# Kernel optimization log

Measured on AMD Instinct MI355X. Metric: run time of the kernel, lower is better.

The kernel has to match this reference:

```python
import jax, jax.numpy as jnp
import numpy as np

N = 50000      # nodes
E = 800000     # edges (before self-loops)
F = 128        # num_features
H = 64         # hidden_channels
B = 512        # batch_size (num graphs)
NC = 10        # num_classes


def setup_inputs() -> dict:
    key = jax.random.key(0)
    ks = jax.random.split(key, 24)
    rn = lambda k, shp, s=0.05: jax.random.normal(k, shp, jnp.float32) * s
    inp = {}
    inp["x"] = jax.random.normal(ks[0], (N, F), jnp.float32)
    inp["edge_index"] = jax.random.randint(ks[1], (2, E), 0, N)
    inp["batch"] = jnp.sort(jax.random.randint(ks[2], (N,), 0, B))
    # GATConv1: in F -> 4 heads x H (concat)
    inp["W1"] = rn(ks[3], (F, 4 * H)); inp["a_src1"] = rn(ks[4], (4, H))
    inp["a_dst1"] = rn(ks[5], (4, H)); inp["b1"] = rn(ks[6], (4 * H,))
    # GATConv2: in 4H -> 1 head x 2H
    inp["W2"] = rn(ks[7], (4 * H, 2 * H)); inp["a_src2"] = rn(ks[8], (1, 2 * H))
    inp["a_dst2"] = rn(ks[9], (1, 2 * H)); inp["b2"] = rn(ks[10], (2 * H,))
    # GCNConv: in 2H -> H
    inp["Wg"] = rn(ks[11], (2 * H, H)); inp["bg"] = rn(ks[12], (H,))
    # BatchNorms (eval mode: running_mean=0, running_var=1)
    inp["bn1_g"] = 1.0 + rn(ks[13], (4 * H,)); inp["bn1_b"] = rn(ks[14], (4 * H,))
    inp["bn2_g"] = 1.0 + rn(ks[15], (2 * H,)); inp["bn2_b"] = rn(ks[16], (2 * H,))
    inp["bn3_g"] = 1.0 + rn(ks[17], (2 * H,)); inp["bn3_b"] = rn(ks[18], (2 * H,))
    inp["lin1_W"] = rn(ks[19], (H, 128)); inp["lin1_b"] = rn(ks[20], (128,))
    inp["lin2_W"] = rn(ks[21], (128, NC)); inp["lin2_b"] = rn(ks[22], (NC,))
    inp["batch_size"] = B
    return inp


def _gat(x, src, dst, W, a_s, a_d, b, n):
    """PyG GATConv (eval): project, edge attention (leaky_relu 0.2), dst-softmax, scatter."""
    heads, ch = a_s.shape
    h = (x @ W).reshape(n, heads, ch)                       # [N, heads, ch]
    sc_s = (h * a_s).sum(-1)                                # [N, heads]
    sc_d = (h * a_d).sum(-1)
    e = jax.nn.leaky_relu(sc_s[src] + sc_d[dst], 0.2)       # [E2, heads]
    m = jax.ops.segment_max(e, dst, num_segments=n)
    ee = jnp.exp(e - m[dst])
    s = jax.ops.segment_sum(ee, dst, num_segments=n)
    alpha = ee / (s[dst] + 1e-16)                           # edge softmax per dst
    out = jax.ops.segment_sum(h[src] * alpha[:, :, None], dst, num_segments=n)
    return out.reshape(n, heads * ch) + b


def _bn_eval(x, g, b, eps=1e-5):
    # BatchNorm1d eval with running_mean=0, running_var=1
    return x * (g / jnp.sqrt(1.0 + eps)) + b


def reference(x, edge_index, batch, W1, a_src1, a_dst1, b1, W2, a_src2, a_dst2, b2,
              Wg, bg, bn1_g, bn1_b, bn2_g, bn2_b, bn3_g, bn3_b,
              lin1_W, lin1_b, lin2_W, lin2_b, batch_size):
    n = x.shape[0]
    loop = jnp.arange(n)
    src = jnp.concatenate([edge_index[0], loop])            # add self-loops (PyG default)
    dst = jnp.concatenate([edge_index[1], loop])
    lrelu = lambda v: jax.nn.leaky_relu(v, 0.01)            # module's LeakyReLU()

    x1 = _bn_eval(lrelu(_gat(x, src, dst, W1, a_src1, a_dst1, b1, n)), bn1_g, bn1_b)
    x2 = _bn_eval(lrelu(_gat(x1, src, dst, W2, a_src2, a_dst2, b2, n)), bn2_g, bn2_b)

    # GCNConv with symmetric normalization over A + I
    deg = jax.ops.segment_sum(jnp.ones_like(dst, jnp.float32), dst, num_segments=n)
    dis = jnp.where(deg > 0, jax.lax.rsqrt(deg), 0.0)
    h = x2 @ Wg                                             # [N, H]
    msg = h[src] * (dis[src] * dis[dst])[:, None]
    x3 = lrelu(jax.ops.segment_sum(msg, dst, num_segments=n) + bg)

    # global_mean_pool over graphs (dropout is identity in eval)
    sums = jax.ops.segment_sum(x3, batch, num_segments=batch_size)
    cnt = jax.ops.segment_sum(jnp.ones((n,), jnp.float32), batch, num_segments=batch_size)
    pooled = sums / jnp.clip(cnt, 1.0)[:, None]             # [B, H]

    y = lrelu(_bn_eval(pooled @ lin1_W + lin1_b, bn3_g, bn3_b))
    return y @ lin2_W + lin2_b                              # [B, NC]
```

## Files before the change

### kernel.cpp

```cpp
#include <hip/hip_runtime.h>
#include <hip/hip_bf16.h>

#define NN  50000
#define EE  800000
#define NE2 850000
#define NB  512
#define NRT 3125
#define NSB 196

#define BN_RS 0.9999950000374997f

typedef __attribute__((ext_vector_type(8))) short short8;
typedef __attribute__((ext_vector_type(4))) float f32x4;

__device__ __forceinline__ float bf2f(__hip_bfloat16 v) { return __bfloat162float(v); }
__device__ __forceinline__ unsigned short f2b(float v) {
    __hip_bfloat16 b = __float2bfloat16(v);
    return *reinterpret_cast<unsigned short*>(&b);
}
__device__ __forceinline__ float u2f(unsigned short u) {
    union { unsigned u; float f; } c; c.u = ((unsigned)u) << 16; return c.f;
}
__device__ __forceinline__ float4 u42f4(ushort4 v) {
    float4 r; r.x = u2f(v.x); r.y = u2f(v.y); r.z = u2f(v.z); r.w = u2f(v.w); return r;
}
__device__ __forceinline__ float lrelu01(float v) { return v > 0.f ? v : 0.01f * v; }
__device__ __forceinline__ float lrelu02(float v) { return v > 0.f ? v : 0.2f * v; }

__device__ __forceinline__ void edge_sd(const int* __restrict__ ei, int e, int& s, int& d) {
    if (e < EE) { s = ei[e]; d = ei[EE + e]; }
    else        { s = e - EE; d = e - EE; }
}

__device__ __forceinline__ float ldf(const void* p, int i, bool bf) {
    return bf ? bf2f(((const __hip_bfloat16*)p)[i]) : ((const float*)p)[i];
}

__global__ __launch_bounds__(256) void det_k(const unsigned* __restrict__ xw, int* __restrict__ flag) {
    __shared__ int cnt;
    if (threadIdx.x == 0) cnt = 0;
    __syncthreads();
    int c = 0;
#pragma unroll
    for (int k = 0; k < 4; ++k) {
        unsigned w = xw[threadIdx.x * 4 + k];
        unsigned ef = (w >> 7) & 0xFFu;
        if (ef >= 100u && ef <= 140u) c++;
    }
    atomicAdd(&cnt, c);
    __syncthreads();
    if (threadIdx.x == 0) *flag = (cnt > 512) ? 1 : 0;
}

#define NSEG 20
#define WTOT 85578
#define XQUADS (NN * 32)
#define PREP_TOT (XQUADS + WTOT + 32768 + 32768 + 8192)
struct SegArgs { const void* src[NSEG]; int off[NSEG]; };

__global__ __launch_bounds__(256) void prep_k(SegArgs a,
                                              const void* __restrict__ x_raw,
                                              ushort4* __restrict__ xb4,
                                              const void* __restrict__ W1r,
                                              const void* __restrict__ W2r,
                                              const void* __restrict__ Wgr,
                                              float* __restrict__ wf,
                                              unsigned short* __restrict__ W1t,
                                              unsigned short* __restrict__ W2t,
                                              unsigned short* __restrict__ Wgt,
                                              const int* __restrict__ flag) {
    bool bf = (*flag != 0);
    int i = blockIdx.x * 256 + threadIdx.x;
    if (i >= PREP_TOT) return;
    if (i < XQUADS) {
        ushort4 o;
        if (bf) o = ((const ushort4*)x_raw)[i];
        else {
            float4 v = ((const float4*)x_raw)[i];
            o.x = f2b(v.x); o.y = f2b(v.y); o.z = f2b(v.z); o.w = f2b(v.w);
        }
        xb4[i] = o;
        return;
    }
    i -= XQUADS;
    if (i < WTOT) {
        int s = 0;
#pragma unroll
        for (int k = 1; k < NSEG; ++k) if (i >= a.off[k]) s = k;
        wf[i] = ldf(a.src[s], i - a.off[s], bf);
        return;
    }
    i -= WTOT;
    if (i < 32768) {
        int n = i >> 7, k = i & 127;
        W1t[i] = f2b(ldf(W1r, k * 256 + n, bf));
        return;
    }
    i -= 32768;
    if (i < 32768) {
        int n = i >> 8, k = i & 255;
        W2t[i] = f2b(ldf(W2r, k * 128 + n, bf));
        return;
    }
    i -= 32768;
    {
        int n = i >> 7, k = i & 127;
        Wgt[i] = f2b(ldf(Wgr, k * 64 + n, bf));
    }
}

__global__ __launch_bounds__(256) void deg_k(const int* __restrict__ ei, int* __restrict__ degi) {
    int e = blockIdx.x * 256 + threadIdx.x;
    if (e >= NE2) return;
    int s, d; edge_sd(ei, e, s, d);
    atomicAdd(&degi[d], 1);
}

__global__ __launch_bounds__(256) void pscan_k(const int* __restrict__ degi,
                                               int* __restrict__ incl, int* __restrict__ bsum) {
    __shared__ int tmp[256];
    int t = threadIdx.x;
    int i = blockIdx.x * 256 + t;
    int v = (i < NN) ? degi[i] : 0;
    tmp[t] = v;
    __syncthreads();
#pragma unroll
    for (int off = 1; off < 256; off <<= 1) {
        int u = (t >= off) ? tmp[t - off] : 0;
        __syncthreads();
        tmp[t] += u;
        __syncthreads();
    }
    if (i < NN) incl[i] = tmp[t];
    if (t == 255) bsum[blockIdx.x] = tmp[255];
}

__global__ __launch_bounds__(256) void bscan_k(int* __restrict__ bsum) {
    __shared__ int tmp[256];
    int t = threadIdx.x;
    tmp[t] = (t < NSB) ? bsum[t] : 0;
    __syncthreads();
#pragma unroll
    for (int off = 1; off < 256; off <<= 1) {
        int u = (t >= off) ? tmp[t - off] : 0;
        __syncthreads();
        tmp[t] += u;
        __syncthreads();
    }
    if (t < NSB) bsum[t] = tmp[t];
}

__global__ __launch_bounds__(256) void fscan_k(const int* __restrict__ degi,
                                               const int* __restrict__ incl,
                                               const int* __restrict__ bsum,
                                               int* __restrict__ row_ptr, int* __restrict__ cursor,
                                               float* __restrict__ dis) {
    int i = blockIdx.x * 256 + threadIdx.x;
    if (i >= NN) return;
    int dg = degi[i];
    int base = (blockIdx.x > 0) ? bsum[blockIdx.x - 1] : 0;
    int ex = base + incl[i] - dg;
    row_ptr[i] = ex; cursor[i] = ex;
    dis[i] = dg > 0 ? rsqrtf((float)dg) : 0.f;
    if (i == NN - 1) row_ptr[NN] = bsum[NSB - 1];
}

__global__ __launch_bounds__(256) void scatter_k(const int* __restrict__ ei,
                                                 int* __restrict__ cursor,
                                                 int* __restrict__ csr_src) {
    int e = blockIdx.x * 256 + threadIdx.x;
    if (e >= NE2) return;
    int s, d; edge_sd(ei, e, s, d);
    int pos = atomicAdd(&cursor[d], 1);
    csr_src[pos] = s;
}

__global__ __launch_bounds__(256) void mgemm1_k(const short* __restrict__ A,
                                                const short* __restrict__ Bt,
                                                unsigned short* __restrict__ C,
                                                const float* __restrict__ a_s,
                                                const float* __restrict__ a_d,
                                                float* __restrict__ sc_s,
                                                float* __restrict__ sc_d) {
    int wave = threadIdx.x >> 6, lane = threadIdx.x & 63;
    int rt = blockIdx.x, cg = wave;
    int l15 = lane & 15, quad = lane >> 4;
    const short* ap = A + (size_t)(rt * 16 + l15) * 128 + quad * 8;
    const short* bp = Bt + (size_t)(cg * 64 + l15) * 128 + quad * 8;
    f32x4 acc[4] = {};
    for (int k0 = 0; k0 < 128; k0 += 32) {
        short8 a = *(const short8*)(ap + k0);
#pragma unroll
        for (int j = 0; j < 4; ++j) {
            short8 b = *(const short8*)(bp + (size_t)j * 16 * 128 + k0);
            acc[j] = __builtin_amdgcn_mfma_f32_16x16x32_bf16(a, b, acc[j], 0, 0, 0);
        }
    }
    float asv[4], adv[4];
#pragma unroll
    for (int j = 0; j < 4; ++j) {
        asv[j] = a_s[cg * 64 + j * 16 + l15];
        adv[j] = a_d[cg * 64 + j * 16 + l15];
    }
    float ss[4] = {0.f, 0.f, 0.f, 0.f}, sd[4] = {0.f, 0.f, 0.f, 0.f};
#pragma unroll
    for (int j = 0; j < 4; ++j) {
        int n = cg * 64 + j * 16 + l15;
#pragma unroll
        for (int r = 0; r < 4; ++r) {
            float v = acc[j][r];
            C[(size_t)(rt * 16 + quad * 4 + r) * 256 + n] = f2b(v);
            ss[r] = fmaf(v, asv[j], ss[r]);
            sd[r] = fmaf(v, adv[j], sd[r]);
        }
    }
#pragma unroll
    for (int off = 1; off < 16; off <<= 1) {
#pragma unroll
        for (int r = 0; r < 4; ++r) {
            ss[r] += __shfl_xor(ss[r], off);
            sd[r] += __shfl_xor(sd[r], off);
        }
    }
    if (l15 == 0) {
#pragma unroll
        for (int r = 0; r < 4; ++r) {
            int node = rt * 16 + quad * 4 + r;
            sc_s[node * 4 + cg] = ss[r];
            sc_d[node * 4 + cg] = sd[r];
        }
    }
}

__global__ __launch_bounds__(256) void mgemm2_k(const short* __restrict__ A,
                                                const short* __restrict__ Bt,
                                                unsigned short* __restrict__ C,
                                                const float* __restrict__ a_s,
                                                const float* __restrict__ a_d,
                                                float* __restrict__ sc_s,
                                                float* __restrict__ sc_d) {
    __shared__ float sred[4][16][2];
    int wave = threadIdx.x >> 6, lane = threadIdx.x & 63;
    int gidx = blockIdx.x * 4 + wave;
    bool act = gidx < NRT * 2;
    int gcl = act ? gidx : NRT * 2 - 1;
    int rt = gcl >> 1, cg = gcl & 1;
    int l15 = lane & 15, quad = lane >> 4;
    const short* ap = A + (size_t)(rt * 16 + l15) * 256 + quad * 8;
    const short* bp = Bt + (size_t)(cg * 64 + l15) * 256 + quad * 8;
    f32x4 acc[4] = {};
    for (int k0 = 0; k0 < 256; k0 += 32) {
        short8 a = *(const short8*)(ap + k0);
#pragma unroll
        for (int j = 0; j < 4; ++j) {
            short8 b = *(const short8*)(bp + (size_t)j * 16 * 256 + k0);
            acc[j] = __builtin_amdgcn_mfma_f32_16x16x32_bf16(a, b, acc[j], 0, 0, 0);
        }
    }
    float asv[4], adv[4];
#pragma unroll
    for (int j = 0; j < 4; ++j) {
        asv[j] = a_s[cg * 64 + j * 16 + l15];
        adv[j] = a_d[cg * 64 + j * 16 + l15];
    }
    float ss[4] = {0.f, 0.f, 0.f, 0.f}, sd[4] = {0.f, 0.f, 0.f, 0.f};
#pragma unroll
    for (int j = 0; j < 4; ++j) {
        int n = cg * 64 + j * 16 + l15;
#pragma unroll
        for (int r = 0; r < 4; ++r) {
            float v = acc[j][r];
            if (act) C[(size_t)(rt * 16 + quad * 4 + r) * 128 + n] = f2b(v);
            ss[r] = fmaf(v, asv[j], ss[r]);
            sd[r] = fmaf(v, adv[j], sd[r]);
        }
    }
#pragma unroll
    for (int off = 1; off < 16; off <<= 1) {
#pragma unroll
        for (int r = 0; r < 4; ++r) {
            ss[r] += __shfl_xor(ss[r], off);
            sd[r] += __shfl_xor(sd[r], off);
        }
    }
    if (l15 == 0) {
#pragma unroll
        for (int r = 0; r < 4; ++r) {
            sred[wave][quad * 4 + r][0] = ss[r];
            sred[wave][quad * 4 + r][1] = sd[r];
        }
    }
    __syncthreads();
    if (threadIdx.x < 32) {
        int rl = threadIdx.x >> 4, row = threadIdx.x & 15;
        int g2 = blockIdx.x * 4 + rl * 2;
        if (g2 < NRT * 2) {
            int node = (g2 >> 1) * 16 + row;
            sc_s[node] = sred[rl * 2][row][0] + sred[rl * 2 + 1][row][0];
            sc_d[node] = sred[rl * 2][row][1] + sred[rl * 2 + 1][row][1];
        }
    }
}

__global__ __launch_bounds__(256) void mgemm3_k(const short* __restrict__ A,
                                                const short* __restrict__ Bt,
                                                unsigned short* __restrict__ C) {
    int wave = threadIdx.x >> 6, lane = threadIdx.x & 63;
    int gidx = blockIdx.x * 4 + wave;
    if (gidx >= NRT) return;
    int rt = gidx;
    int l15 = lane & 15, quad = lane >> 4;
    const short* ap = A + (size_t)(rt * 16 + l15) * 128 + quad * 8;
    const short* bp = Bt + (size_t)l15 * 128 + quad * 8;
    f32x4 acc[4] = {};
    for (int k0 = 0; k0 < 128; k0 += 32) {
        short8 a = *(const short8*)(ap + k0);
#pragma unroll
        for (int j = 0; j < 4; ++j) {
            short8 b = *(const short8*)(bp + (size_t)j * 16 * 128 + k0);
            acc[j] = __builtin_amdgcn_mfma_f32_16x16x32_bf16(a, b, acc[j], 0, 0, 0);
        }
    }
#pragma unroll
    for (int j = 0; j < 4; ++j) {
        int n = j * 16 + l15;
#pragma unroll
        for (int r = 0; r < 4; ++r)
            C[(size_t)(rt * 16 + quad * 4 + r) * 64 + n] = f2b(acc[j][r]);
    }
}

__device__ __forceinline__ float sel4(float4 v, int head) {
    float ab = (head & 1) ? v.y : v.x;
    float cd = (head & 1) ? v.w : v.z;
    return (head & 2) ? cd : ab;
}

__global__ __launch_bounds__(256) void agg1_k(const int* __restrict__ row_ptr,
                                              const int* __restrict__ csr_src,
                                              const ushort4* __restrict__ h1b,
                                              const float4* __restrict__ sc_s4,
                                              const float4* __restrict__ sc_d4,
                                              const float4* __restrict__ b1,
                                              const float4* __restrict__ g1,
                                              const float4* __restrict__ bb1,
                                              ushort4* __restrict__ x1b) {
    int n = __builtin_amdgcn_readfirstlane((blockIdx.x * 256 + threadIdx.x) >> 6);
    int lane = threadIdx.x & 63;
    if (n >= NN) return;
    int row = row_ptr[n], end = row_ptr[n + 1];
    int head = lane >> 4;
    float scd_h = sel4(sc_d4[n], head);
    float4 acc = {0.f, 0.f, 0.f, 0.f};
    float den = 0.f;
    int c = row;
    for (; c + 3 < end; c += 4) {
        int s0 = csr_src[c], s1 = csr_src[c + 1], s2 = csr_src[c + 2], s3 = csr_src[c + 3];
        float4 scs0 = sc_s4[s0], scs1 = sc_s4[s1], scs2 = sc_s4[s2], scs3 = sc_s4[s3];
        float4 hv0 = u42f4(h1b[(size_t)s0 * 64 + lane]);
        float4 hv1 = u42f4(h1b[(size_t)s1 * 64 + lane]);
        float4 hv2 = u42f4(h1b[(size_t)s2 * 64 + lane]);
        float4 hv3 = u42f4(h1b[(size_t)s3 * 64 + lane]);
        float e0 = __expf(lrelu02(sel4(scs0, head) + scd_h));
        float e1 = __expf(lrelu02(sel4(scs1, head) + scd_h));
        float e2 = __expf(lrelu02(sel4(scs2, head) + scd_h));
        float e3 = __expf(lrelu02(sel4(scs3, head) + scd_h));
        den += (e0 + e1) + (e2 + e3);
        acc.x = fmaf(hv0.x, e0, fmaf(hv1.x, e1, fmaf(hv2.x, e2, fmaf(hv3.x, e3, acc.x))));
        acc.y = fmaf(hv0.y, e0, fmaf(hv1.y, e1, fmaf(hv2.y, e2, fmaf(hv3.y, e3, acc.y))));
        acc.z = fmaf(hv0.z, e0, fmaf(hv1.z, e1, fmaf(hv2.z, e2, fmaf(hv3.z, e3, acc.z))));
        acc.w = fmaf(hv0.w, e0, fmaf(hv1.w, e1, fmaf(hv2.w, e2, fmaf(hv3.w, e3, acc.w))));
    }
    for (; c < end; ++c) {
        int s0 = csr_src[c];
        float4 scs0 = sc_s4[s0];
        float4 hv0 = u42f4(h1b[(size_t)s0 * 64 + lane]);
        float e0 = __expf(lrelu02(sel4(scs0, head) + scd_h));
        den += e0;
        acc.x = fmaf(hv0.x, e0, acc.x);
        acc.y = fmaf(hv0.y, e0, acc.y);
        acc.z = fmaf(hv0.z, e0, acc.z);
        acc.w = fmaf(hv0.w, e0, acc.w);
    }
    float inv = 1.f / (den + 1e-16f);
    float4 bb = b1[lane], gg = g1[lane], be = bb1[lane];
    ushort4 o;
    o.x = f2b(lrelu01(acc.x * inv + bb.x) * (gg.x * BN_RS) + be.x);
    o.y = f2b(lrelu01(acc.y * inv + bb.y) * (gg.y * BN_RS) + be.y);
    o.z = f2b(lrelu01(acc.z * inv + bb.z) * (gg.z * BN_RS) + be.z);
    o.w = f2b(lrelu01(acc.w * inv + bb.w) * (gg.w * BN_RS) + be.w);
    x1b[(size_t)n * 64 + lane] = o;
}

__global__ __launch_bounds__(256) void agg2_k(const int* __restrict__ row_ptr,
                                              const int* __restrict__ csr_src,
                                              const ushort4* __restrict__ h2b,
                                              const float* __restrict__ sc_s,
                                              const float* __restrict__ sc_d,
                                              const float4* __restrict__ b2,
                                              const float4* __restrict__ g2,
                                              const float4* __restrict__ bb2,
                                              ushort4* __restrict__ x2b) {
    int n = __builtin_amdgcn_readfirstlane((blockIdx.x * 256 + threadIdx.x) >> 6);
    int lane = threadIdx.x & 63;
    if (n >= NN) return;
    int g = lane >> 5, sl = lane & 31;
    int row = row_ptr[n], end = row_ptr[n + 1];
    float scd = sc_d[n];
    float4 acc = {0.f, 0.f, 0.f, 0.f};
    float den = 0.f;
    int c = row + g;
    for (; c + 2 < end; c += 4) {
        int s0 = csr_src[c], s1 = csr_src[c + 2];
        float sc0 = sc_s[s0], sc1 = sc_s[s1];
        float4 hv0 = u42f4(h2b[(size_t)s0 * 32 + sl]);
        float4 hv1 = u42f4(h2b[(size_t)s1 * 32 + sl]);
        float e0 = __expf(lrelu02(sc0 + scd));
        float e1 = __expf(lrelu02(sc1 + scd));
        den += e0 + e1;
        acc.x = fmaf(hv0.x, e0, fmaf(hv1.x, e1, acc.x));
        acc.y = fmaf(hv0.y, e0, fmaf(hv1.y, e1, acc.y));
        acc.z = fmaf(hv0.z, e0, fmaf(hv1.z, e1, acc.z));
        acc.w = fmaf(hv0.w, e0, fmaf(hv1.w, e1, acc.w));
    }
    if (c < end) {
        int s0 = csr_src[c];
        float e0 = __expf(lrelu02(sc_s[s0] + scd));
        float4 hv0 = u42f4(h2b[(size_t)s0 * 32 + sl]);
        den += e0;
        acc.x = fmaf(hv0.x, e0, acc.x);
        acc.y = fmaf(hv0.y, e0, acc.y);
        acc.z = fmaf(hv0.z, e0, acc.z);
        acc.w = fmaf(hv0.w, e0, acc.w);
    }
    den += __shfl_xor(den, 32);
    acc.x += __shfl_xor(acc.x, 32);
    acc.y += __shfl_xor(acc.y, 32);
    acc.z += __shfl_xor(acc.z, 32);
    acc.w += __shfl_xor(acc.w, 32);
    if (g == 0) {
        float inv = 1.f / (den + 1e-16f);
        float4 bb = b2[sl], gg = g2[sl], be = bb2[sl];
        ushort4 o;
        o.x = f2b(lrelu01(acc.x * inv + bb.x) * (gg.x * BN_RS) + be.x);
        o.y = f2b(lrelu01(acc.y * inv + bb.y) * (gg.y * BN_RS) + be.y);
        o.z = f2b(lrelu01(acc.z * inv + bb.z) * (gg.z * BN_RS) + be.z);
        o.w = f2b(lrelu01(acc.w * inv + bb.w) * (gg.w * BN_RS) + be.w);
        x2b[(size_t)n * 32 + sl] = o;
    }
}

__global__ __launch_bounds__(256) void gcn_k(const int* __restrict__ row_ptr,
                                             const int* __restrict__ csr_src,
                                             const ushort4* __restrict__ hgb,
                                             const float* __restrict__ dis,
                                             const float4* __restrict__ bg,
                                             float4* __restrict__ x3) {
    int n = __builtin_amdgcn_readfirstlane((blockIdx.x * 256 + threadIdx.x) >> 6);
    int lane = threadIdx.x & 63;
    if (n >= NN) return;
    int g = lane >> 4, sl = lane & 15;
    int row = row_ptr[n], end = row_ptr[n + 1];
    float dn = dis[n];
    float4 acc = {0.f, 0.f, 0.f, 0.f};
    int c = row + g;
    for (; c + 4 < end; c += 8) {
        int s0 = csr_src[c], s1 = csr_src[c + 4];
        float w0 = dis[s0], w1 = dis[s1];
        float4 hv0 = u42f4(hgb[(size_t)s0 * 16 + sl]);
        float4 hv1 = u42f4(hgb[(size_t)s1 * 16 + sl]);
        acc.x = fmaf(hv0.x, w0, fmaf(hv1.x, w1, acc.x));
        acc.y = fmaf(hv0.y, w0, fmaf(hv1.y, w1, acc.y));
        acc.z = fmaf(hv0.z, w0, fmaf(hv1.z, w1, acc.z));
        acc.w = fmaf(hv0.w, w0, fmaf(hv1.w, w1, acc.w));
    }
    if (c < end) {
        int s0 = csr_src[c];
        float w0 = dis[s0];
        float4 hv0 = u42f4(hgb[(size_t)s0 * 16 + sl]);
        acc.x = fmaf(hv0.x, w0, acc.x);
        acc.y = fmaf(hv0.y, w0, acc.y);
        acc.z = fmaf(hv0.z, w0, acc.z);
        acc.w = fmaf(hv0.w, w0, acc.w);
    }
#pragma unroll
    for (int off = 16; off <= 32; off <<= 1) {
        acc.x += __shfl_xor(acc.x, off);
        acc.y += __shfl_xor(acc.y, off);
        acc.z += __shfl_xor(acc.z, off);
        acc.w += __shfl_xor(acc.w, off);
    }
    if (g == 0) {
        float4 bb = bg[sl];
        float4 o;
        o.x = lrelu01(acc.x * dn + bb.x);
        o.y = lrelu01(acc.y * dn + bb.y);
        o.z = lrelu01(acc.z * dn + bb.z);
        o.w = lrelu01(acc.w * dn + bb.w);
        x3[(size_t)n * 16 + sl] = o;
    }
}

__global__ __launch_bounds__(1024) void bounds_k(const int* __restrict__ batch, int* __restrict__ gstart) {
    int t = threadIdx.x;
    if (t > NB) return;
    int lo = 0, hi = NN;
    while (lo < hi) { int mid = (lo + hi) >> 1; if (batch[mid] < t) lo = mid + 1; else hi = mid; }
    gstart[t] = lo;
}

__global__ __launch_bounds__(256) void pool_k(const float* __restrict__ x3,
                                              const int* __restrict__ gstart,
                                              float* __restrict__ pooled) {
    __shared__ float red[4][64];
    int g = blockIdx.x, t = threadIdx.x;
    int c = t & 63, r = t >> 6;
    int s = gstart[g], e = gstart[g + 1];
    float sum = 0.f;
    for (int n = s + r; n < e; n += 4) sum += x3[(size_t)n * 64 + c];
    red[r][c] = sum;
    __syncthreads();
    if (t < 64) {
        float v = red[0][t] + red[1][t] + red[2][t] + red[3][t];
        int cnt = e - s; if (cnt < 1) cnt = 1;
        pooled[g * 64 + t] = v / (float)cnt;
    }
}

__global__ __launch_bounds__(128) void mlp_k(const float* __restrict__ pooled,
                                             const float* __restrict__ l1W,
                                             const float* __restrict__ l1b,
                                             const float* __restrict__ g3,
                                             const float* __restrict__ b3,
                                             const float* __restrict__ l2W,
                                             const float* __restrict__ l2b,
                                             void* __restrict__ outp,
                                             const int* __restrict__ flag) {
    __shared__ float pl[64];
    __shared__ float y1s[128];
    int g = blockIdx.x, t = threadIdx.x;
    if (t < 64) pl[t] = pooled[g * 64 + t];
    __syncthreads();
    float acc = l1b[t];
#pragma unroll 8
    for (int j = 0; j < 64; ++j) acc = fmaf(pl[j], l1W[j * 128 + t], acc);
    acc = acc * (g3[t] * BN_RS) + b3[t];
    y1s[t] = lrelu01(acc);
    __syncthreads();
    if (t < 10) {
        float o = l2b[t];
#pragma unroll 8
        for (int j = 0; j < 128; ++j) o = fmaf(y1s[j], l2W[j * 10 + t], o);
        if (*flag) ((__hip_bfloat16*)outp)[g * 10 + t] = __float2bfloat16(o);
        else       ((float*)outp)[g * 10 + t] = o;
    }
}

static const int kSegN[NSEG]  = {32768, 256, 256, 256, 32768, 128, 128, 128, 8192, 64,
                                 256, 256, 128, 128, 128, 128, 8192, 128, 1280, 10};
static const int kSegIn[NSEG] = {3, 4, 5, 6, 7, 8, 9, 10, 11, 12, 13, 14, 15, 16, 17, 18, 19, 20, 21, 22};

extern "C" void kernel_launch(void* const* d_in, const int* in_sizes, int n_in,
                              void* d_out, int out_size, void* d_ws, size_t ws_size,
                              hipStream_t stream) {
    const void* x_raw = d_in[0];
    const int*  ei    = (const int*)d_in[1];
    const int*  batch = (const int*)d_in[2];

    int*   flag = (int*)d_ws;
    float* ws   = (float*)d_ws;
    unsigned short* xb = (unsigned short*)(ws + 16);
    float* wf   = ws + 16 + (size_t)NN * 64;
    unsigned short* W1t = (unsigned short*)(wf + 85584);
    unsigned short* W2t = W1t + 32768;
    unsigned short* Wgt = W2t + 32768;
    unsigned short* h1b = Wgt + 8192;
    unsigned short* x1b = h1b + (size_t)NN * 256;
    unsigned short* x2b = x1b + (size_t)NN * 256;
    unsigned short* hgb = x2b + (size_t)NN * 128;
    float* x3   = (float*)(hgb + (size_t)NN * 64);
    float* sc_s1 = x3 + (size_t)NN * 64;
    float* sc_d1 = sc_s1 + (size_t)NN * 4;
    float* sc_s2 = sc_d1 + (size_t)NN * 4;
    float* sc_d2 = sc_s2 + NN;
    float* disb  = sc_d2 + NN;
    float* pooled = disb + NN;
    int*   gstart = (int*)(pooled + NB * 64);
    int*   degi   = gstart + NB + 4;
    int*   incl   = degi + NN;
    int*   bsum   = incl + NN;
    int*   row_ptr = bsum + 256;
    int*   cursor  = row_ptr + NN + 1;
    int*   csr_src = cursor + NN;

    int off[NSEG]; int o = 0;
    for (int s = 0; s < NSEG; ++s) { off[s] = o; o += kSegN[s]; }
    float* as1f = wf + off[1];  float* ad1f = wf + off[2];
    float* b1f  = wf + off[3];  float* as2f = wf + off[5];
    float* ad2f = wf + off[6];  float* b2f  = wf + off[7];
    float* bgf  = wf + off[9];  float* bn1g = wf + off[10]; float* bn1b = wf + off[11];
    float* bn2g = wf + off[12]; float* bn2b = wf + off[13]; float* bn3g = wf + off[14];
    float* bn3b = wf + off[15]; float* l1Wf = wf + off[16]; float* l1bf = wf + off[17];
    float* l2Wf = wf + off[18]; float* l2bf = wf + off[19];

    unsigned short* h2b = h1b;

    det_k<<<1, 256, 0, stream>>>((const unsigned*)x_raw, flag);
    SegArgs sa;
    for (int s = 0; s < NSEG; ++s) { sa.src[s] = d_in[kSegIn[s]]; sa.off[s] = off[s]; }
    prep_k<<<(PREP_TOT + 255) / 256, 256, 0, stream>>>(sa, x_raw, (ushort4*)xb,
                                                       d_in[3], d_in[7], d_in[11],
                                                       wf, W1t, W2t, Wgt, flag);

    hipMemsetAsync(degi, 0, NN * sizeof(int), stream);
    deg_k<<<(NE2 + 255) / 256, 256, 0, stream>>>(ei, degi);
    pscan_k<<<NSB, 256, 0, stream>>>(degi, incl, bsum);
    bscan_k<<<1, 256, 0, stream>>>(bsum);
    fscan_k<<<NSB, 256, 0, stream>>>(degi, incl, bsum, row_ptr, cursor, disb);
    scatter_k<<<(NE2 + 255) / 256, 256, 0, stream>>>(ei, cursor, csr_src);
    bounds_k<<<1, 1024, 0, stream>>>(batch, gstart);

    mgemm1_k<<<NRT, 256, 0, stream>>>((const short*)xb, (const short*)W1t, h1b,
                                      as1f, ad1f, sc_s1, sc_d1);
    agg1_k<<<12500, 256, 0, stream>>>(row_ptr, csr_src, (const ushort4*)h1b,
                                      (const float4*)sc_s1, (const float4*)sc_d1,
                                      (const float4*)b1f, (const float4*)bn1g,
                                      (const float4*)bn1b, (ushort4*)x1b);

    mgemm2_k<<<(NRT * 2 + 3) / 4, 256, 0, stream>>>((const short*)x1b, (const short*)W2t, h2b,
                                                    as2f, ad2f, sc_s2, sc_d2);
    agg2_k<<<12500, 256, 0, stream>>>(row_ptr, csr_src, (const ushort4*)h2b,
                                      sc_s2, sc_d2,
                                      (const float4*)b2f, (const float4*)bn2g,
                                      (const float4*)bn2b, (ushort4*)x2b);

    mgemm3_k<<<(NRT + 3) / 4, 256, 0, stream>>>((const short*)x2b, (const short*)Wgt, hgb);
    gcn_k<<<12500, 256, 0, stream>>>(row_ptr, csr_src, (const ushort4*)hgb, disb,
                                     (const float4*)bgf, (float4*)x3);
    pool_k<<<NB, 256, 0, stream>>>(x3, gstart, pooled);

    mlp_k<<<NB, 128, 0, stream>>>(pooled, l1Wf, l1bf, bn3g, bn3b, l2Wf, l2bf, d_out, flag);
}
```

Baseline: 458.9 us.

## Fold setup kernels into prep and fscan, deepen gather unrolling in aggregations

Merges the dtype-detection kernel and the degree memset into prep_k: every block recomputes the bf16 detection locally and also zeroes degi. It moves the graph-boundary binary search into fscan_k, which cuts three launches. The aggregation loops in agg1/agg2/gcn now issue more independent gathers per iteration, giving more memory-level parallelism. In exchange, every prep block repeats the 1024-word detection read, and the wider unroll raises register pressure.

Measured after the change: 455.9 us. No clear change (-0.6%).

```diff
diff --git a/kernel.cpp b/kernel.cpp
--- a/kernel.cpp
+++ b/kernel.cpp
@@ -36,26 +36,10 @@
     return bf ? bf2f(((const __hip_bfloat16*)p)[i]) : ((const float*)p)[i];
 }
 
-__global__ __launch_bounds__(256) void det_k(const unsigned* __restrict__ xw, int* __restrict__ flag) {
-    __shared__ int cnt;
-    if (threadIdx.x == 0) cnt = 0;
-    __syncthreads();
-    int c = 0;
-#pragma unroll
-    for (int k = 0; k < 4; ++k) {
-        unsigned w = xw[threadIdx.x * 4 + k];
-        unsigned ef = (w >> 7) & 0xFFu;
-        if (ef >= 100u && ef <= 140u) c++;
-    }
-    atomicAdd(&cnt, c);
-    __syncthreads();
-    if (threadIdx.x == 0) *flag = (cnt > 512) ? 1 : 0;
-}
-
 #define NSEG 20
 #define WTOT 85578
 #define XQUADS (NN * 32)
-#define PREP_TOT (XQUADS + WTOT + 32768 + 32768 + 8192)
+#define PREP_TOT (NN + XQUADS + WTOT + 32768 + 32768 + 8192)
 struct SegArgs { const void* src[NSEG]; int off[NSEG]; };
 
 __global__ __launch_bounds__(256) void prep_k(SegArgs a,
@@ -68,10 +52,31 @@
                                               unsigned short* __restrict__ W1t,
                                               unsigned short* __restrict__ W2t,
                                               unsigned short* __restrict__ Wgt,
-                                              const int* __restrict__ flag) {
-    bool bf = (*flag != 0);
-    int i = blockIdx.x * 256 + threadIdx.x;
+                                              int* __restrict__ degi,
+                                              int* __restrict__ flag) {
+    __shared__ int cnt;
+    int t = threadIdx.x;
+    if (t == 0) cnt = 0;
+    __syncthreads();
+    {
+        int c = 0;
+        const unsigned* xw = (const unsigned*)x_raw;
+#pragma unroll
+        for (int k = 0; k < 4; ++k) {
+            unsigned w = xw[t * 4 + k];
+            unsigned ef = (w >> 7) & 0xFFu;
+            if (ef >= 100u && ef <= 140u) c++;
+        }
+        atomicAdd(&cnt, c);
+    }
+    __syncthreads();
+    bool bf = (cnt > 512);
+    if (blockIdx.x == 0 && t == 0) *flag = bf ? 1 : 0;
+
+    int i = blockIdx.x * 256 + t;
     if (i >= PREP_TOT) return;
+    if (i < NN) { degi[i] = 0; return; }
+    i -= NN;
     if (i < XQUADS) {
         ushort4 o;
         if (bf) o = ((const ushort4*)x_raw)[i];
@@ -153,9 +158,15 @@
 __global__ __launch_bounds__(256) void fscan_k(const int* __restrict__ degi,
                                                const int* __restrict__ incl,
                                                const int* __restrict__ bsum,
+                                               const int* __restrict__ batch,
                                                int* __restrict__ row_ptr, int* __restrict__ cursor,
-                                               float* __restrict__ dis) {
+                                               float* __restrict__ dis, int* __restrict__ gstart) {
     int i = blockIdx.x * 256 + threadIdx.x;
+    if (i <= NB) {
+        int lo = 0, hi = NN;
+        while (lo < hi) { int mid = (lo + hi) >> 1; if (batch[mid] < i) lo = mid + 1; else hi = mid; }
+        gstart[i] = lo;
+    }
     if (i >= NN) return;
     int dg = degi[i];
     int base = (blockIdx.x > 0) ? bsum[blockIdx.x - 1] : 0;
@@ -354,22 +365,48 @@
     float4 acc = {0.f, 0.f, 0.f, 0.f};
     float den = 0.f;
     int c = row;
+    for (; c + 7 < end; c += 8) {
+        int s[8];
+#pragma unroll
+        for (int j = 0; j < 8; ++j) s[j] = csr_src[c + j];
+        float4 scs[8];
+#pragma unroll
+        for (int j = 0; j < 8; ++j) scs[j] = sc_s4[s[j]];
+        ushort4 hu[8];
+#pragma unroll
+        for (int j = 0; j < 8; ++j) hu[j] = h1b[(size_t)s[j] * 64 + lane];
+        float e[8];
+#pragma unroll
+        for (int j = 0; j < 8; ++j) { e[j] = __expf(lrelu02(sel4(scs[j], head) + scd_h)); den += e[j]; }
+#pragma unroll
+        for (int j = 0; j < 8; ++j) {
+            float4 hv = u42f4(hu[j]);
+            acc.x = fmaf(hv.x, e[j], acc.x);
+            acc.y = fmaf(hv.y, e[j], acc.y);
+            acc.z = fmaf(hv.z, e[j], acc.z);
+            acc.w = fmaf(hv.w, e[j], acc.w);
+        }
+    }
     for (; c + 3 < end; c += 4) {
-        int s0 = csr_src[c], s1 = csr_src[c + 1], s2 = csr_src[c + 2], s3 = csr_src[c + 3];
-        float4 scs0 = sc_s4[s0], scs1 = sc_s4[s1], scs2 = sc_s4[s2], scs3 = sc_s4[s3];
-        float4 hv0 = u42f4(h1b[(size_t)s0 * 64 + lane]);
-        float4 hv1 = u42f4(h1b[(size_t)s1 * 64 + lane]);
-        float4 hv2 = u42f4(h1b[(size_t)s2 * 64 + lane]);
-        float4 hv3 = u42f4(h1b[(size_t)s3 * 64 + lane]);
-        float e0 = __expf(lrelu02(sel4(scs0, head) + scd_h));
-        float e1 = __expf(lrelu02(sel4(scs1, head) + scd_h));
-        float e2 = __expf(lrelu02(sel4(scs2, head) + scd_h));
-        float e3 = __expf(lrelu02(sel4(scs3, head) + scd_h));
-        den += (e0 + e1) + (e2 + e3);
-        acc.x = fmaf(hv0.x, e0, fmaf(hv1.x, e1, fmaf(hv2.x, e2, fmaf(hv3.x, e3, acc.x))));
-        acc.y = fmaf(hv0.y, e0, fmaf(hv1.y, e1, fmaf(hv2.y, e2, fmaf(hv3.y, e3, acc.y))));
-        acc.z = fmaf(hv0.z, e0, fmaf(hv1.z, e1, fmaf(hv2.z, e2, fmaf(hv3.z, e3, acc.z))));
-        acc.w = fmaf(hv0.w, e0, fmaf(hv1.w, e1, fmaf(hv2.w, e2, fmaf(hv3.w, e3, acc.w))));
+        int s[4];
+#pragma unroll
+        for (int j = 0; j < 4; ++j) s[j] = csr_src[c + j];
+        float4 scs[4];
+#pragma unroll
+        for (int j = 0; j < 4; ++j) scs[j] = sc_s4[s[j]];
+        ushort4 hu[4];
+#pragma unroll
+        for (int j = 0; j < 4; ++j) hu[j] = h1b[(size_t)s[j] * 64 + lane];
+#pragma unroll
+        for (int j = 0; j < 4; ++j) {
+            float e0 = __expf(lrelu02(sel4(scs[j], head) + scd_h));
+            den += e0;
+            float4 hv = u42f4(hu[j]);
+            acc.x = fmaf(hv.x, e0, acc.x);
+            acc.y = fmaf(hv.y, e0, acc.y);
+            acc.z = fmaf(hv.z, e0, acc.z);
+            acc.w = fmaf(hv.w, e0, acc.w);
+        }
     }
     for (; c < end; ++c) {
         int s0 = csr_src[c];
@@ -410,20 +447,28 @@
     float4 acc = {0.f, 0.f, 0.f, 0.f};
     float den = 0.f;
     int c = row + g;
-    for (; c + 2 < end; c += 4) {
-        int s0 = csr_src[c], s1 = csr_src[c + 2];
-        float sc0 = sc_s[s0], sc1 = sc_s[s1];
-        float4 hv0 = u42f4(h2b[(size_t)s0 * 32 + sl]);
-        float4 hv1 = u42f4(h2b[(size_t)s1 * 32 + sl]);
-        float e0 = __expf(lrelu02(sc0 + scd));
-        float e1 = __expf(lrelu02(sc1 + scd));
-        den += e0 + e1;
-        acc.x = fmaf(hv0.x, e0, fmaf(hv1.x, e1, acc.x));
-        acc.y = fmaf(hv0.y, e0, fmaf(hv1.y, e1, acc.y));
-        acc.z = fmaf(hv0.z, e0, fmaf(hv1.z, e1, acc.z));
-        acc.w = fmaf(hv0.w, e0, fmaf(hv1.w, e1, acc.w));
-    }
-    if (c < end) {
+    for (; c + 6 < end; c += 8) {
+        int s[4];
+#pragma unroll
+        for (int j = 0; j < 4; ++j) s[j] = csr_src[c + 2 * j];
+        float sc[4];
+#pragma unroll
+        for (int j = 0; j < 4; ++j) sc[j] = sc_s[s[j]];
+        ushort4 hu[4];
+#pragma unroll
+        for (int j = 0; j < 4; ++j) hu[j] = h2b[(size_t)s[j] * 32 + sl];
+#pragma unroll
+        for (int j = 0; j < 4; ++j) {
+            float e0 = __expf(lrelu02(sc[j] + scd));
+            den += e0;
+            float4 hv = u42f4(hu[j]);
+            acc.x = fmaf(hv.x, e0, acc.x);
+            acc.y = fmaf(hv.y, e0, acc.y);
+            acc.z = fmaf(hv.z, e0, acc.z);
+            acc.w = fmaf(hv.w, e0, acc.w);
+        }
+    }
+    for (; c < end; c += 2) {
         int s0 = csr_src[c];
         float e0 = __expf(lrelu02(sc_s[s0] + scd));
         float4 hv0 = u42f4(h2b[(size_t)s0 * 32 + sl]);
@@ -464,17 +509,26 @@
     float dn = dis[n];
     float4 acc = {0.f, 0.f, 0.f, 0.f};
     int c = row + g;
-    for (; c + 4 < end; c += 8) {
-        int s0 = csr_src[c], s1 = csr_src[c + 4];
-        float w0 = dis[s0], w1 = dis[s1];
-        float4 hv0 = u42f4(hgb[(size_t)s0 * 16 + sl]);
-        float4 hv1 = u42f4(hgb[(size_t)s1 * 16 + sl]);
-        acc.x = fmaf(hv0.x, w0, fmaf(hv1.x, w1, acc.x));
-        acc.y = fmaf(hv0.y, w0, fmaf(hv1.y, w1, acc.y));
-        acc.z = fmaf(hv0.z, w0, fmaf(hv1.z, w1, acc.z));
-        acc.w = fmaf(hv0.w, w0, fmaf(hv1.w, w1, acc.w));
-    }
-    if (c < end) {
+    for (; c + 12 < end; c += 16) {
+        int s[4];
+#pragma unroll
+        for (int j = 0; j < 4; ++j) s[j] = csr_src[c + 4 * j];
+        float w[4];
+#pragma unroll
+        for (int j = 0; j < 4; ++j) w[j] = dis[s[j]];
+        ushort4 hu[4];
+#pragma unroll
+        for (int j = 0; j < 4; ++j) hu[j] = hgb[(size_t)s[j] * 16 + sl];
+#pragma unroll
+        for (int j = 0; j < 4; ++j) {
+            float4 hv = u42f4(hu[j]);
+            acc.x = fmaf(hv.x, w[j], acc.x);
+            acc.y = fmaf(hv.y, w[j], acc.y);
+            acc.z = fmaf(hv.z, w[j], acc.z);
+            acc.w = fmaf(hv.w, w[j], acc.w);
+        }
+    }
+    for (; c < end; c += 4) {
         int s0 = csr_src[c];
         float w0 = dis[s0];
         float4 hv0 = u42f4(hgb[(size_t)s0 * 16 + sl]);
@@ -499,14 +553,6 @@
         o.w = lrelu01(acc.w * dn + bb.w);
         x3[(size_t)n * 16 + sl] = o;
     }
-}
-
-__global__ __launch_bounds__(1024) void bounds_k(const int* __restrict__ batch, int* __restrict__ gstart) {
-    int t = threadIdx.x;
-    if (t > NB) return;
-    int lo = 0, hi = NN;
-    while (lo < hi) { int mid = (lo + hi) >> 1; if (batch[mid] < t) lo = mid + 1; else hi = mid; }
-    gstart[t] = lo;
 }
 
 __global__ __launch_bounds__(256) void pool_k(const float* __restrict__ x3,
@@ -605,20 +651,17 @@
 
     unsigned short* h2b = h1b;
 
-    det_k<<<1, 256, 0, stream>>>((const unsigned*)x_raw, flag);
     SegArgs sa;
     for (int s = 0; s < NSEG; ++s) { sa.src[s] = d_in[kSegIn[s]]; sa.off[s] = off[s]; }
     prep_k<<<(PREP_TOT + 255) / 256, 256, 0, stream>>>(sa, x_raw, (ushort4*)xb,
                                                        d_in[3], d_in[7], d_in[11],
-                                                       wf, W1t, W2t, Wgt, flag);
-
-    hipMemsetAsync(degi, 0, NN * sizeof(int), stream);
+                                                       wf, W1t, W2t, Wgt, degi, flag);
+
     deg_k<<<(NE2 + 255) / 256, 256, 0, stream>>>(ei, degi);
     pscan_k<<<NSB, 256, 0, stream>>>(degi, incl, bsum);
     bscan_k<<<1, 256, 0, stream>>>(bsum);
-    fscan_k<<<NSB, 256, 0, stream>>>(degi, incl, bsum, row_ptr, cursor, disb);
+    fscan_k<<<NSB, 256, 0, stream>>>(degi, incl, bsum, batch, row_ptr, cursor, disb, gstart);
     scatter_k<<<(NE2 + 255) / 256, 256, 0, stream>>>(ei, cursor, csr_src);
-    bounds_k<<<1, 1024, 0, stream>>>(batch, gstart);
 
     mgemm1_k<<<NRT, 256, 0, stream>>>((const short*)xb, (const short*)W1t, h1b,
                                       as1f, ad1f, sc_s1, sc_d1);
```
